# Performance work log

Measured on AMD Instinct MI355X. Metric: run time of the kernel, lower is better.

Reference implementation:

```python
import jax, jax.numpy as jnp
import numpy as np

NUM_HEADS = 8
IN_CH = 256  # C per branch; x has 2*C channels
DHW = (16, 16, 16)


def _proj(w, b, feat):
    # 1x1x1 Conv3d == per-voxel linear over channels. w: [Co, Ci], feat: [B, Ci, D, H, W]
    return jnp.einsum('oc,bcdhw->bodhw', w, feat) + b[None, :, None, None, None]


def _rope(n, dim):
    # matches rotary_embedding: returns [dim, n]
    inv_freq = 1.0 / (10000.0 ** (jnp.arange(0, dim, 2, dtype=jnp.float32) / dim))
    pos = jnp.linspace(-1.0, 1.0, n)
    sinusoid = pos[:, None] * inv_freq[None, :]          # [n, dim//2]
    emb = jnp.concatenate([jnp.sin(sinusoid), jnp.cos(sinusoid)], axis=-1)  # [n, dim]
    return emb.T                                          # [dim, n]


def setup_inputs() -> dict:
    key = jax.random.key(0)
    ks = jax.random.split(key, 5)
    D, H, W = DHW
    C = IN_CH
    s = 0.05
    return {
        'x': jax.random.normal(ks[0], (1, 2 * C, D, H, W), dtype=jnp.float32),
        'wq': jax.random.normal(ks[1], (C, C), dtype=jnp.float32) * s,
        'bq': jnp.zeros((C,), jnp.float32),
        'wk': jax.random.normal(ks[2], (C, C), dtype=jnp.float32) * s,
        'bk': jnp.zeros((C,), jnp.float32),
        'wv': jax.random.normal(ks[3], (C, C), dtype=jnp.float32) * s,
        'bv': jnp.zeros((C,), jnp.float32),
        'wo': jax.random.normal(ks[4], (2 * C, C), dtype=jnp.float32) * s,
        'bo': jnp.zeros((2 * C,), jnp.float32),
    }


def reference(x, wq, bq, wk, bk, wv, bv, wo, bo):
    qf, kvf = jnp.split(x, 2, axis=1)          # each [B, C, D, H, W]
    B, C, D, H, W = qf.shape
    hd = C // NUM_HEADS
    N = D * H * W
    q = _proj(wq, bq, qf).reshape(B, NUM_HEADS, hd, N)
    k = _proj(wk, bk, kvf).reshape(B, NUM_HEADS, hd, N)
    v = _proj(wv, bv, kvf).reshape(B, NUM_HEADS, hd, N)
    pe = _rope(N, hd)                           # [hd, N]
    q = q * pe[None, None]
    k = k * pe[None, None]
    attn = jnp.einsum('bhcn,bhcm->bhnm', q, k)  # note: no 1/sqrt(d) scaling, as in source
    attn = jax.nn.softmax(attn, axis=-1)
    out = jnp.einsum('bhnm,bhcm->bhcn', attn, v).reshape(B, C, D, H, W)
    return _proj(wo, bo, out + qf)              # [B, 2C, D, H, W]
```

## Files before the change

kernel.cpp:

```cpp
#include <hip/hip_runtime.h>
#include <hip/hip_bf16.h>

#define CIN 256
#define NV 4096
#define NHEAD 8
#define HD 32
#define NSPLIT 4
#define KSPAN (NV / NSPLIT)
#define LOG2E 1.44269504088896340736f
#define LOG2_10K_16 0.8304820237218405f

typedef __attribute__((ext_vector_type(8))) short short8;
typedef __attribute__((ext_vector_type(4))) float f32x4;

static __device__ __forceinline__ unsigned short f2bf(float f) {
    union { float f; unsigned u; } v; v.f = f;
    unsigned r = v.u + 0x7fffu + ((v.u >> 16) & 1u);
    return (unsigned short)(r >> 16);
}
static __device__ __forceinline__ unsigned pk_bf2(float x0, float x1) {
    return __builtin_amdgcn_perm(__float_as_uint(x1), __float_as_uint(x0),
                                 0x07060302u);
}
static __device__ __forceinline__ float bflo(unsigned u) {
    return __uint_as_float(u << 16);
}
static __device__ __forceinline__ float bfhi(unsigned u) {
    return __uint_as_float(u & 0xffff0000u);
}

__global__ __launch_bounds__(256) void conv_w(
    const float* __restrict__ wq, const float* __restrict__ wk,
    const float* __restrict__ wv, const float* __restrict__ wo,
    unsigned short* __restrict__ Wb)
{
    int i = (blockIdx.x * 256 + threadIdx.x) * 4;
    if (i >= 327680) return;
    const float* src;
    int off = i;
    if (i < 65536) { src = wq; }
    else if (i < 131072) { src = wk; off = i - 65536; }
    else if (i < 196608) { src = wv; off = i - 131072; }
    else { src = wo; off = i - 196608; }
    float4 v = *(const float4*)&src[off];
    unsigned short pk[4] = {f2bf(v.x), f2bf(v.y), f2bf(v.z), f2bf(v.w)};
    *(uint2*)&Wb[i] = *(uint2*)pk;
}

__global__ __launch_bounds__(512) void qkv_fused(
    const float* __restrict__ x, const unsigned short* __restrict__ Wb,
    const float* __restrict__ bq, const float* __restrict__ bk,
    const float* __restrict__ bv,
    unsigned short* __restrict__ Qbf, unsigned short* __restrict__ Kbf,
    unsigned short* __restrict__ Vbf)
{
    const int which = blockIdx.z;
    const unsigned short* Wp = Wb + (size_t)which * 65536;
    const float* Bp = (which == 0) ? bq : (which == 1) ? bk : bv;
    const int cbase = (which == 0) ? 0 : CIN;

    const int n0 = blockIdx.x * 32;
    const int m0 = blockIdx.y * 128;
    const int t = threadIdx.x;

    __shared__ __align__(16) unsigned short Sbuf[32 * 264];

    {
        const int n = t & 31, cg = t >> 5;
#pragma unroll 4
        for (int cc = 0; cc < 16; cc += 2) {
            const int c = cg * 16 + cc;
            size_t off = (size_t)(cbase + c) * NV + n0 + n;
            *(unsigned*)&Sbuf[n * 264 + c] = pk_bf2(x[off], x[off + NV]);
        }
    }
    __syncthreads();

    const int w = t >> 6;
    const int lane = t & 63;
    const int ln = lane & 15;
    const int quad = lane >> 4;
    const int M = m0 + w * 16 + ln;

    f32x4 acc[2] = {};
    const unsigned short* Wrow = &Wp[(size_t)M * 256 + quad * 8];
    for (int k0 = 0; k0 < 256; k0 += 32) {
        short8 a = *(const short8*)&Wrow[k0];
        short8 b[2];
#pragma unroll
        for (int nt = 0; nt < 2; ++nt)
            b[nt] = *(const short8*)&Sbuf[(nt * 16 + ln) * 264 + k0 + quad * 8];
        if (which == 2) {
#pragma unroll
            for (int nt = 0; nt < 2; ++nt)
                acc[nt] = __builtin_amdgcn_mfma_f32_16x16x32_bf16(
                    b[nt], a, acc[nt], 0, 0, 0);
        } else {
#pragma unroll
            for (int nt = 0; nt < 2; ++nt)
                acc[nt] = __builtin_amdgcn_mfma_f32_16x16x32_bf16(
                    a, b[nt], acc[nt], 0, 0, 0);
        }
    }
    __syncthreads();

    if (which == 2) {
        const int cl = w * 16 + ln;
        const float bias = Bp[m0 + cl];
#pragma unroll
        for (int nt = 0; nt < 2; ++nt) {
            unsigned short pk4[4];
#pragma unroll
            for (int r = 0; r < 4; ++r) pk4[r] = f2bf(acc[nt][r] + bias);
            *(uint2*)&Sbuf[cl * 40 + nt * 16 + quad * 4] = *(uint2*)pk4;
        }
        __syncthreads();
        {
            const int cl2 = t >> 2, q = t & 3;
            uint2 lo = *(const uint2*)&Sbuf[cl2 * 40 + q * 4];
            uint2 hi = *(const uint2*)&Sbuf[cl2 * 40 + 16 + q * 4];
            uint4 v;
            v.x = lo.x; v.y = lo.y; v.z = hi.x; v.w = hi.y;
            *(uint4*)&Vbf[(size_t)(m0 + cl2) * NV + n0 + q * 8] = v;
        }
    } else {
        const int mb = m0 + w * 16 + quad * 4;
        const int cb = mb & 31;
        const float qscale = (which == 0) ? LOG2E : 1.0f;
        float bias[4], invf[4];
#pragma unroll
        for (int r = 0; r < 4; ++r) {
            bias[r] = Bp[mb + r];
            invf[r] = __builtin_amdgcn_exp2f(
                -(float)((cb + r) & 15) * LOG2_10K_16);
        }
        const bool use_sin = (cb < 16);
        const int ml = w * 16 + quad * 4;
#pragma unroll
        for (int nt = 0; nt < 2; ++nt) {
            const int n = n0 + nt * 16 + ln;
            const float pos = (float)n * (2.0f / 4095.0f) - 1.0f;
#pragma unroll
            for (int r = 0; r < 4; ++r) {
                float ang = pos * invf[r];
                float f = (use_sin ? __sinf(ang) : __cosf(ang)) * qscale;
                Sbuf[(nt * 16 + ln) * 264 + ml + r] =
                    f2bf((acc[nt][r] + bias[r]) * f);
            }
        }
        __syncthreads();
        unsigned short* dst = (which == 0) ? Qbf : Kbf;
        const int h0 = m0 >> 5;
        {
            const int hh = t >> 7;
            const int n = (t >> 2) & 31;
            const int cw = t & 3;
            uint4 v = *(const uint4*)&Sbuf[n * 264 + hh * 32 + cw * 8];
            *(uint4*)&dst[((size_t)(h0 + hh) * NV + n0 + n) * HD + cw * 8] = v;
        }
    }
}

__global__ __launch_bounds__(256, 4) void attn_mfma(
    const unsigned short* __restrict__ Qbf,
    const unsigned short* __restrict__ Kbf,
    const unsigned short* __restrict__ Vbf,
    unsigned short* __restrict__ Opartb, float* __restrict__ Lpart)
{
    const int l = blockIdx.x + (blockIdx.y << 6) + (blockIdx.z << 9);
    const int pr = l & 31;
    const int h = pr & 7;
    const int z = pr >> 3;
    const int q0 = (l >> 5) * 64;
    const int kbase = z * KSPAN;
    const int t = threadIdx.x;
    const int w = t >> 6;
    const int lane = t & 63;
    const int ln = lane & 15;
    const int quad = lane >> 4;

    __shared__ __align__(16) unsigned short Ks[2 * 4096];
    __shared__ __align__(16) unsigned short Vs[2 * 4096];

    const short8 qa = *(const short8*)
        &Qbf[((size_t)h * NV + q0 + w * 16 + ln) * HD + quad * 8];

    const unsigned short* Kh = Kbf + (size_t)h * NV * HD;
    const unsigned short* Vh = Vbf + (size_t)h * HD * NV;

    const int cv = t >> 3;
    const unsigned short* gsrcV = Vh + (size_t)cv * NV + ((t & 7) ^ (cv & 7)) * 8;
    const int kv = t >> 2;
    const unsigned short* gsrcK =
        Kh + (size_t)kv * HD + ((t & 3) ^ (kv & 3)) * 8;

    f32x4 oacc[2] = {};
    f32x4 lacc = {};
    const short vone = (short)0x3F80;
    const short8 vones = {vone, vone, vone, vone, vone, vone, vone, vone};

    __builtin_amdgcn_global_load_lds(
        (const __attribute__((address_space(1))) unsigned int*)(gsrcK +
            (size_t)kbase * HD),
        (__attribute__((address_space(3))) unsigned int*)&Ks[t * 8], 16, 0, 0);
    __builtin_amdgcn_global_load_lds(
        (const __attribute__((address_space(1))) unsigned int*)(gsrcK +
            (size_t)(kbase + 64) * HD),
        (__attribute__((address_space(3))) unsigned int*)&Ks[2048 + t * 8],
        16, 0, 0);
    __builtin_amdgcn_global_load_lds(
        (const __attribute__((address_space(1))) unsigned int*)(gsrcV + kbase),
        (__attribute__((address_space(3))) unsigned int*)&Vs[t * 8], 16, 0, 0);
    __builtin_amdgcn_global_load_lds(
        (const __attribute__((address_space(1))) unsigned int*)(gsrcV + kbase +
            64),
        (__attribute__((address_space(3))) unsigned int*)&Vs[2048 + t * 8],
        16, 0, 0);
    __syncthreads();

    const int sgk = (quad ^ (ln & 3)) * 8;
    for (int i = 0; i < KSPAN / 128; ++i) {
        const int kb = kbase + i * 128;
        const int buf = (i & 1) * 4096;

        if (i + 1 < KSPAN / 128) {
            const int nb = buf ^ 4096;
            __builtin_amdgcn_global_load_lds(
                (const __attribute__((address_space(1))) unsigned int*)(gsrcK +
                    (size_t)(kb + 128) * HD),
                (__attribute__((address_space(3))) unsigned int*)&Ks[nb + t * 8],
                16, 0, 0);
            __builtin_amdgcn_global_load_lds(
                (const __attribute__((address_space(1))) unsigned int*)(gsrcK +
                    (size_t)(kb + 192) * HD),
                (__attribute__((address_space(3))) unsigned int*)&Ks[nb + 2048 +
                    t * 8],
                16, 0, 0);
            __builtin_amdgcn_global_load_lds(
                (const __attribute__((address_space(1))) unsigned int*)(gsrcV +
                    kb + 128),
                (__attribute__((address_space(3))) unsigned int*)&Vs[nb + t * 8],
                16, 0, 0);
            __builtin_amdgcn_global_load_lds(
                (const __attribute__((address_space(1))) unsigned int*)(gsrcV +
                    kb + 192),
                (__attribute__((address_space(3))) unsigned int*)&Vs[nb + 2048 +
                    t * 8],
                16, 0, 0);
        }

#pragma unroll
        for (int hf = 0; hf < 2; ++hf) {
            const int sb = buf + hf * 2048;

            f32x4 s[4];
            __builtin_amdgcn_s_setprio(1);
#pragma unroll
            for (int ct = 0; ct < 4; ++ct) {
                const short8 kf = *(const short8*)
                    &Ks[sb + (ct * 16 + ln) * 32 + sgk];
                f32x4 z4 = {0.f, 0.f, 0.f, 0.f};
                s[ct] = __builtin_amdgcn_mfma_f32_16x16x32_bf16(kf, qa, z4,
                                                                0, 0, 0);
            }
            __builtin_amdgcn_s_setprio(0);

            float p[4][4];
#pragma unroll
            for (int ct = 0; ct < 4; ++ct)
#pragma unroll
                for (int r = 0; r < 4; ++r)
                    p[ct][r] = __builtin_amdgcn_exp2f(s[ct][r]);

#pragma unroll
            for (int h2 = 0; h2 < 2; ++h2) {
                short8 pa;
                unsigned* pau = (unsigned*)&pa;
                pau[0] = pk_bf2(p[2 * h2][0], p[2 * h2][1]);
                pau[1] = pk_bf2(p[2 * h2][2], p[2 * h2][3]);
                pau[2] = pk_bf2(p[2 * h2 + 1][0], p[2 * h2 + 1][1]);
                pau[3] = pk_bf2(p[2 * h2 + 1][2], p[2 * h2 + 1][3]);
                __builtin_amdgcn_s_setprio(1);
                lacc = __builtin_amdgcn_mfma_f32_16x16x32_bf16(pa, vones, lacc,
                                                               0, 0, 0);
#pragma unroll
                for (int ctile = 0; ctile < 2; ++ctile) {
                    const int cA = ctile * 16 + ln;
                    const short8 vb = *(const short8*)
                        &Vs[sb + cA * 64 + (((h2 * 4 + quad) ^ (cA & 7)) * 8)];
                    oacc[ctile] = __builtin_amdgcn_mfma_f32_16x16x32_bf16(
                        pa, vb, oacc[ctile], 0, 0, 0);
                }
                __builtin_amdgcn_s_setprio(0);
            }
        }
        __syncthreads();
    }

    unsigned short* Oz = Opartb + (size_t)z * CIN * NV;
    float* Lz = Lpart + (size_t)z * NHEAD * NV;
    if (ln == 0) {
#pragma unroll
        for (int r = 0; r < 4; ++r)
            Lz[(size_t)h * NV + q0 + w * 16 + quad * 4 + r] = lacc[r];
    }
#pragma unroll
    for (int ctile = 0; ctile < 2; ++ctile) {
        uint2 st;
        st.x = pk_bf2(oacc[ctile][0], oacc[ctile][1]);
        st.y = pk_bf2(oacc[ctile][2], oacc[ctile][3]);
        *(uint2*)&Oz[(size_t)(h * HD + ctile * 16 + ln) * NV + q0 + w * 16 +
                     quad * 4] = st;
    }
}

__global__ __launch_bounds__(512) void out_fused(
    const float* __restrict__ x,
    const unsigned short* __restrict__ Opartb,
    const float* __restrict__ Lpart,
    const unsigned short* __restrict__ Wob, const float* __restrict__ bo,
    float* __restrict__ out)
{
    const int n0 = blockIdx.x * 32;
    const int m0 = blockIdx.y * 128;
    const int t = threadIdx.x;

    __shared__ __align__(16) unsigned short Ys[32 * 264];

    {
        const int n2 = (t & 15) * 2;
        const int grp = t >> 4;
        const int h = grp >> 2;
        const size_t lo = (size_t)h * NV + n0 + n2;
        float l0 = 0.f, l1 = 0.f;
#pragma unroll
        for (int zz = 0; zz < NSPLIT; ++zz) {
            l0 += Lpart[(size_t)zz * NHEAD * NV + lo];
            l1 += Lpart[(size_t)zz * NHEAD * NV + lo + 1];
        }
        const float rl0 = __builtin_amdgcn_rcpf(l0);
        const float rl1 = __builtin_amdgcn_rcpf(l1);
#pragma unroll
        for (int i = 0; i < 8; ++i) {
            const int c = grp * 8 + i;
            size_t off = (size_t)c * NV + n0 + n2;
            float s0 = 0.f, s1 = 0.f;
#pragma unroll
            for (int zz = 0; zz < NSPLIT; ++zz) {
                unsigned o = *(const unsigned*)&Opartb[(size_t)zz * CIN * NV + off];
                s0 += bflo(o);
                s1 += bfhi(o);
            }
            float2 x2 = *(const float2*)&x[off];
            Ys[n2 * 264 + c] = f2bf(s0 * rl0 + x2.x);
            Ys[(n2 + 1) * 264 + c] = f2bf(s1 * rl1 + x2.y);
        }
    }
    __syncthreads();

    const int w = t >> 6;
    const int lane = t & 63;
    const int ln = lane & 15;
    const int quad = lane >> 4;
    const int M = m0 + w * 16 + ln;

    const unsigned short* Wrow = &Wob[(size_t)M * 256 + quad * 8];
    f32x4 acc[2] = {};
    for (int k0 = 0; k0 < 256; k0 += 32) {
        short8 a = *(const short8*)&Wrow[k0];
        short8 b[2];
#pragma unroll
        for (int nt = 0; nt < 2; ++nt)
            b[nt] = *(const short8*)&Ys[(nt * 16 + ln) * 264 + k0 + quad * 8];
#pragma unroll
        for (int nt = 0; nt < 2; ++nt)
            acc[nt] = __builtin_amdgcn_mfma_f32_16x16x32_bf16(
                a, b[nt], acc[nt], 0, 0, 0);
    }

    const int mb = m0 + w * 16 + quad * 4;
    float bias[4];
#pragma unroll
    for (int r = 0; r < 4; ++r) bias[r] = bo[mb + r];
#pragma unroll
    for (int nt = 0; nt < 2; ++nt)
#pragma unroll
        for (int r = 0; r < 4; ++r)
            out[(size_t)(mb + r) * NV + n0 + nt * 16 + ln] =
                acc[nt][r] + bias[r];
}

extern "C" void kernel_launch(void* const* d_in, const int* in_sizes, int n_in,
                              void* d_out, int out_size, void* d_ws,
                              size_t ws_size, hipStream_t stream)
{
    const float* x  = (const float*)d_in[0];
    const float* wq = (const float*)d_in[1];
    const float* bq = (const float*)d_in[2];
    const float* wk = (const float*)d_in[3];
    const float* bk = (const float*)d_in[4];
    const float* wv = (const float*)d_in[5];
    const float* bv = (const float*)d_in[6];
    const float* wo = (const float*)d_in[7];
    const float* bo = (const float*)d_in[8];
    float* out = (float*)d_out;

    unsigned short* Wb  = (unsigned short*)d_ws;
    unsigned short* Qbf = Wb + 327680;
    unsigned short* Kbf = Qbf + (size_t)CIN * NV;
    unsigned short* Vbf = Kbf + (size_t)CIN * NV;
    float* Lpart = (float*)(Vbf + (size_t)CIN * NV);
    unsigned short* Opartb =
        (unsigned short*)(Lpart + NSPLIT * (size_t)NHEAD * NV);

    conv_w<<<dim3(320), 256, 0, stream>>>(wq, wk, wv, wo, Wb);
    qkv_fused<<<dim3(128, 2, 3), 512, 0, stream>>>(
        x, Wb, bq, bk, bv, Qbf, Kbf, Vbf);
    attn_mfma<<<dim3(NV / 64, NHEAD, NSPLIT), 256, 0, stream>>>(
        Qbf, Kbf, Vbf, Opartb, Lpart);
    out_fused<<<dim3(128, 4), 512, 0, stream>>>(
        x, Opartb, Lpart, Wb + 196608, bo, out);
}
```

Before: 122.2 us.

## Split key tiles across warps and reduce partial attention outputs in LDS

Each warp now owns all 64 query rows of the block but only a quarter of each 128-key tile, instead of 16 query rows over all keys. K and V fragments are loaded from LDS once per tile and reused across four query tiles, cutting LDS read traffic per MFMA. At the end, the per-warp partial O and row sums are combined through shared memory. This adds a reduction pass and more accumulator registers (4x oacc), which may reduce occupancy under the 256x4 launch bound.

```diff
diff --git a/kernel.cpp b/kernel.cpp
--- a/kernel.cpp
+++ b/kernel.cpp
@@ -179,11 +179,15 @@
     const int ln = lane & 15;
     const int quad = lane >> 4;
 
-    __shared__ __align__(16) unsigned short Ks[2 * 4096];
-    __shared__ __align__(16) unsigned short Vs[2 * 4096];
-
-    const short8 qa = *(const short8*)
-        &Qbf[((size_t)h * NV + q0 + w * 16 + ln) * HD + quad * 8];
+    __shared__ __align__(16) char Smem[33792];
+    unsigned short* Ks = (unsigned short*)Smem;
+    unsigned short* Vs = (unsigned short*)(Smem + 16384);
+
+    short8 qa[4];
+#pragma unroll
+    for (int qt = 0; qt < 4; ++qt)
+        qa[qt] = *(const short8*)
+            &Qbf[((size_t)h * NV + q0 + qt * 16 + ln) * HD + quad * 8];
 
     const unsigned short* Kh = Kbf + (size_t)h * NV * HD;
     const unsigned short* Vh = Vbf + (size_t)h * HD * NV;
@@ -194,8 +198,8 @@
     const unsigned short* gsrcK =
         Kh + (size_t)kv * HD + ((t & 3) ^ (kv & 3)) * 8;
 
-    f32x4 oacc[2] = {};
-    f32x4 lacc = {};
+    f32x4 oacc[4][2] = {};
+    f32x4 lacc[4] = {};
     const short vone = (short)0x3F80;
     const short8 vones = {vone, vone, vone, vone, vone, vone, vone, vone};
 
@@ -219,6 +223,9 @@
     __syncthreads();
 
     const int sgk = (quad ^ (ln & 3)) * 8;
+    const int wsub = (w >> 1) * 2048;
+    const int wh = w & 1;
+
     for (int i = 0; i < KSPAN / 128; ++i) {
         const int kb = kbase + i * 128;
         const int buf = (i & 1) * 4096;
@@ -249,52 +256,71 @@
                 16, 0, 0);
         }
 
-#pragma unroll
-        for (int hf = 0; hf < 2; ++hf) {
-            const int sb = buf + hf * 2048;
-
-            f32x4 s[4];
+        const unsigned short* Kb = &Ks[buf + wsub];
+        const unsigned short* Vb = &Vs[buf + wsub];
+        const short8 kf0 = *(const short8*)&Kb[(wh * 32 + ln) * 32 + sgk];
+        const short8 kf1 = *(const short8*)&Kb[(wh * 32 + 16 + ln) * 32 + sgk];
+        const int cA0 = ln, cA1 = 16 + ln;
+        const short8 vb0 = *(const short8*)
+            &Vb[cA0 * 64 + (((wh * 4 + quad) ^ (cA0 & 7)) * 8)];
+        const short8 vb1 = *(const short8*)
+            &Vb[cA1 * 64 + (((wh * 4 + quad) ^ (cA1 & 7)) * 8)];
+
+#pragma unroll
+        for (int qt = 0; qt < 4; ++qt) {
+            f32x4 z4 = {0.f, 0.f, 0.f, 0.f};
             __builtin_amdgcn_s_setprio(1);
-#pragma unroll
-            for (int ct = 0; ct < 4; ++ct) {
-                const short8 kf = *(const short8*)
-                    &Ks[sb + (ct * 16 + ln) * 32 + sgk];
-                f32x4 z4 = {0.f, 0.f, 0.f, 0.f};
-                s[ct] = __builtin_amdgcn_mfma_f32_16x16x32_bf16(kf, qa, z4,
-                                                                0, 0, 0);
+            f32x4 s0 = __builtin_amdgcn_mfma_f32_16x16x32_bf16(kf0, qa[qt],
+                                                               z4, 0, 0, 0);
+            f32x4 s1 = __builtin_amdgcn_mfma_f32_16x16x32_bf16(kf1, qa[qt],
+                                                               z4, 0, 0, 0);
+            __builtin_amdgcn_s_setprio(0);
+
+            float p0[4], p1[4];
+#pragma unroll
+            for (int r = 0; r < 4; ++r) {
+                p0[r] = __builtin_amdgcn_exp2f(s0[r]);
+                p1[r] = __builtin_amdgcn_exp2f(s1[r]);
             }
+            short8 pa;
+            unsigned* pau = (unsigned*)&pa;
+            pau[0] = pk_bf2(p0[0], p0[1]);
+            pau[1] = pk_bf2(p0[2], p0[3]);
+            pau[2] = pk_bf2(p1[0], p1[1]);
+            pau[3] = pk_bf2(p1[2], p1[3]);
+
+            __builtin_amdgcn_s_setprio(1);
+            lacc[qt] = __builtin_amdgcn_mfma_f32_16x16x32_bf16(pa, vones,
+                                                               lacc[qt],
+                                                               0, 0, 0);
+            oacc[qt][0] = __builtin_amdgcn_mfma_f32_16x16x32_bf16(
+                pa, vb0, oacc[qt][0], 0, 0, 0);
+            oacc[qt][1] = __builtin_amdgcn_mfma_f32_16x16x32_bf16(
+                pa, vb1, oacc[qt][1], 0, 0, 0);
             __builtin_amdgcn_s_setprio(0);
-
-            float p[4][4];
-#pragma unroll
-            for (int ct = 0; ct < 4; ++ct)
-#pragma unroll
-                for (int r = 0; r < 4; ++r)
-                    p[ct][r] = __builtin_amdgcn_exp2f(s[ct][r]);
-
-#pragma unroll
-            for (int h2 = 0; h2 < 2; ++h2) {
-                short8 pa;
-                unsigned* pau = (unsigned*)&pa;
-                pau[0] = pk_bf2(p[2 * h2][0], p[2 * h2][1]);
-                pau[1] = pk_bf2(p[2 * h2][2], p[2 * h2][3]);
-                pau[2] = pk_bf2(p[2 * h2 + 1][0], p[2 * h2 + 1][1]);
-                pau[3] = pk_bf2(p[2 * h2 + 1][2], p[2 * h2 + 1][3]);
-                __builtin_amdgcn_s_setprio(1);
-                lacc = __builtin_amdgcn_mfma_f32_16x16x32_bf16(pa, vones, lacc,
-                                                               0, 0, 0);
-#pragma unroll
-                for (int ctile = 0; ctile < 2; ++ctile) {
-                    const int cA = ctile * 16 + ln;
-                    const short8 vb = *(const short8*)
-                        &Vs[sb + cA * 64 + (((h2 * 4 + quad) ^ (cA & 7)) * 8)];
-                    oacc[ctile] = __builtin_amdgcn_mfma_f32_16x16x32_bf16(
-                        pa, vb, oacc[ctile], 0, 0, 0);
-                }
-                __builtin_amdgcn_s_setprio(0);
-            }
         }
         __syncthreads();
+    }
+
+    float* Ored = (float*)Smem;
+    float* lred = (float*)(Smem + 32768);
+#pragma unroll
+    for (int qt = 0; qt < 4; ++qt) {
+#pragma unroll
+        for (int ct = 0; ct < 2; ++ct)
+            *(f32x4*)&Ored[(((w * 4 + qt) * 2 + ct) << 8) + lane * 4] =
+                oacc[qt][ct];
+        if (ln == 0)
+            *(f32x4*)&lred[(w * 4 + qt) * 16 + quad * 4] = lacc[qt];
+    }
+    __syncthreads();
+
+    f32x4 of0 = {}, of1 = {}, lf = {};
+#pragma unroll
+    for (int w2 = 0; w2 < 4; ++w2) {
+        of0 += *(const f32x4*)&Ored[(((w2 * 4 + w) * 2 + 0) << 8) + lane * 4];
+        of1 += *(const f32x4*)&Ored[(((w2 * 4 + w) * 2 + 1) << 8) + lane * 4];
+        lf  += *(const f32x4*)&lred[(w2 * 4 + w) * 16 + quad * 4];
     }
 
     unsigned short* Oz = Opartb + (size_t)z * CIN * NV;
@@ -302,14 +328,16 @@
     if (ln == 0) {
 #pragma unroll
         for (int r = 0; r < 4; ++r)
-            Lz[(size_t)h * NV + q0 + w * 16 + quad * 4 + r] = lacc[r];
-    }
-#pragma unroll
-    for (int ctile = 0; ctile < 2; ++ctile) {
+            Lz[(size_t)h * NV + q0 + w * 16 + quad * 4 + r] = lf[r];
+    }
+    {
         uint2 st;
-        st.x = pk_bf2(oacc[ctile][0], oacc[ctile][1]);
-        st.y = pk_bf2(oacc[ctile][2], oacc[ctile][3]);
-        *(uint2*)&Oz[(size_t)(h * HD + ctile * 16 + ln) * NV + q0 + w * 16 +
+        st.x = pk_bf2(of0[0], of0[1]);
+        st.y = pk_bf2(of0[2], of0[3]);
+        *(uint2*)&Oz[(size_t)(h * HD + ln) * NV + q0 + w * 16 + quad * 4] = st;
+        st.x = pk_bf2(of1[0], of1[1]);
+        st.y = pk_bf2(of1[2], of1[3]);
+        *(uint2*)&Oz[(size_t)(h * HD + 16 + ln) * NV + q0 + w * 16 +
                      quad * 4] = st;
     }
 }
```

New measurement: 121.7 us. About the same (-0.4%).
